# Performance work log

Measured on AMD Instinct MI355X. Metric: run time of the kernel, lower is better.

Reference implementation:

```python
import jax, jax.numpy as jnp
import numpy as np

NUM_FILTER = 256
CAPS_LEN = 8
NUM_EMOTIONS = 8
OUT_DIM = 16
NUM_CHANNEL = 25
TIME_LEN = 25
NUM_CAPS = NUM_CHANNEL * TIME_LEN * (NUM_FILTER // CAPS_LEN)  # 20000
NUM_ITERATIONS = 3


def setup_inputs() -> dict:
    key = jax.random.key(0)
    ks = jax.random.split(key, 10)
    B = 32
    x = jax.random.normal(ks[0], (B, 54, 54), jnp.float32)
    conv1_w = jax.random.normal(ks[1], (NUM_FILTER, 1, 6, 6), jnp.float32) * 0.05
    conv1_b = jax.random.normal(ks[2], (NUM_FILTER,), jnp.float32) * 0.01
    conv2_w = jax.random.normal(ks[3], (NUM_FILTER, NUM_FILTER, 6, 6), jnp.float32) * 0.01
    conv2_b = jax.random.normal(ks[4], (NUM_FILTER,), jnp.float32) * 0.01
    conv3_w = jax.random.normal(ks[5], (NUM_FILTER, 2 * NUM_FILTER, 1, 1), jnp.float32) * 0.05
    conv3_b = jax.random.normal(ks[6], (NUM_FILTER,), jnp.float32) * 0.01
    # PrimaryCaps: one Linear(caps_len -> caps_len) per capsule, batched as [nc, out, in]
    pc_w = jax.random.normal(ks[7], (NUM_CAPS, CAPS_LEN, CAPS_LEN), jnp.float32) * 0.1
    pc_b = jax.random.normal(ks[8], (NUM_CAPS, CAPS_LEN), jnp.float32) * 0.1
    # EmotionCaps transform W: [nc, num_emotions, out_dim, in_dim]
    W = jax.random.normal(ks[9], (NUM_CAPS, NUM_EMOTIONS, OUT_DIM, CAPS_LEN), jnp.float32) * 0.05
    return {"x": x, "conv1_w": conv1_w, "conv1_b": conv1_b, "conv2_w": conv2_w,
            "conv2_b": conv2_b, "conv3_w": conv3_w, "conv3_b": conv3_b,
            "pc_w": pc_w, "pc_b": pc_b, "W": W}


def _conv(x, w, b, stride):
    y = jax.lax.conv_general_dilated(x, w, (stride, stride), 'VALID',
                                     dimension_numbers=('NCHW', 'OIHW', 'NCHW'))
    return y + b[None, :, None, None]


def _squash(s):
    # scale = |s|^2 / (1 + |s|^2); out = scale * s / (|s| + 1e-8)
    n2 = jnp.sum(s * s, axis=-1, keepdims=True)
    n = jnp.sqrt(n2)
    return (n2 / (1.0 + n2)) * s / (n + 1e-8)


def reference(x, conv1_w, conv1_b, conv2_w, conv2_b, conv3_w, conv3_b, pc_w, pc_b, W):
    x4 = x[:, None]                                    # [B,1,54,54]
    x1 = jax.nn.relu(_conv(x4, conv1_w, conv1_b, 2))   # [B,F,25,25]
    y = jnp.pad(x1, ((0, 0), (0, 0), (2, 3), (2, 3)))  # ZeroPad2d((2,3,2,3))
    y = jax.nn.relu(_conv(y, conv2_w, conv2_b, 1))     # [B,F,25,25]
    z = jax.nn.relu(jnp.concatenate([x1, y], axis=1))  # [B,2F,25,25]
    z = _conv(z, conv3_w, conv3_b, 1)                  # [B,F,25,25]
    B, F, H, Wd = z.shape
    # flatten to capsules: [B, F//caps_len, caps_len, H*W] -> [B, nc, caps_len]
    caps = z.reshape(B, F // CAPS_LEN, CAPS_LEN, H * Wd)
    caps = caps.transpose(0, 1, 3, 2).reshape(B, NUM_CAPS, CAPS_LEN)
    # PrimaryCaps: per-capsule linear, batched as a single einsum
    u = jnp.einsum('bni,noi->bno', caps, pc_w) + pc_b[None]   # [B,nc,caps_len]
    # EmotionCaps: u_hat[b,n,e,o] = W[n,e,o,i] u[b,n,i]
    u_hat = jnp.einsum('bni,neoi->bneo', u, W)                # [B,nc,ne,out_dim]
    b = jnp.zeros((B, NUM_CAPS, NUM_EMOTIONS), u.dtype)
    v = None
    for r in range(NUM_ITERATIONS):
        c = jax.nn.softmax(b, axis=2)[..., None]              # [B,nc,ne,1]
        v = _squash(jnp.sum(c * u_hat, axis=1))               # [B,ne,out_dim]
        if r < NUM_ITERATIONS - 1:
            b = b + jnp.einsum('bneo,beo->bne', u_hat, v)
    return jnp.linalg.norm(v, axis=-1)                        # [B,ne]
```

## Files before the change

kernel.cpp:

```cpp
#include <hip/hip_runtime.h>
#include <hip/hip_fp16.h>

typedef unsigned short u16;
typedef __attribute__((ext_vector_type(8))) short bf16x8;
typedef __attribute__((ext_vector_type(4))) float floatx4;
typedef __attribute__((ext_vector_type(2))) _Float16 half2v;

#define NPIX 625
#define NCAPS 20000
#define K2 9216

__device__ __forceinline__ u16 f2bf(float f) {
  unsigned u = __float_as_uint(f);
  return (u16)((u + 0x7fffu + ((u >> 16) & 1u)) >> 16);
}

__device__ __forceinline__ unsigned h16(float f) {
  union { _Float16 h; u16 b; } c;
  c.h = (_Float16)f;
  return (unsigned)c.b;
}

__device__ __forceinline__ half2v as_h2(unsigned u) {
  union { unsigned i; half2v h; } c;
  c.i = u;
  return c.h;
}

__device__ __forceinline__ float dot2f(unsigned a, unsigned b, float c) {
#if __has_builtin(__builtin_amdgcn_fdot2)
  return __builtin_amdgcn_fdot2(as_h2(a), as_h2(b), c, false);
#else
  half2v x = as_h2(a), y = as_h2(b);
  return fmaf((float)x[1], (float)y[1], fmaf((float)x[0], (float)y[0], c));
#endif
}

__device__ __forceinline__ float dotrow16(uint4 w, uint4 u) {
  float s = dot2f(w.x, u.x, 0.f);
  s = dot2f(w.y, u.y, s);
  s = dot2f(w.z, u.z, s);
  s = dot2f(w.w, u.w, s);
  return s;
}

__device__ __forceinline__ float dot8v(float4 a0, float4 a1, float4 b0, float4 b1) {
  float s = a0.x * b0.x;
  s = fmaf(a0.y, b0.y, s); s = fmaf(a0.z, b0.z, s); s = fmaf(a0.w, b0.w, s);
  s = fmaf(a1.x, b1.x, s); s = fmaf(a1.y, b1.y, s);
  s = fmaf(a1.z, b1.z, s); s = fmaf(a1.w, b1.w, s);
  return s;
}

#define GLDS16(g, l) __builtin_amdgcn_global_load_lds( \
    (const __attribute__((address_space(1))) void*)(g), \
    (__attribute__((address_space(3))) void*)(l), 16, 0, 0)

#define MFMA16(a, b, c) __builtin_amdgcn_mfma_f32_16x16x32_bf16((a), (b), (c), 0, 0, 0)

__global__ void prep_conv1(const float* __restrict__ w2, const float* __restrict__ w3,
                           u16* __restrict__ A2c, u16* __restrict__ A3,
                           const float* __restrict__ x, const float* __restrict__ w1,
                           const float* __restrict__ b1, u16* __restrict__ x1p) {
  if (blockIdx.x < 256) {
    const int oc = blockIdx.x, c = threadIdx.x;
    const float* src = w2 + (oc * 256 + c) * 36;
    float v[36];
#pragma unroll
    for (int k = 0; k < 9; k++) {
      const float4 q = *(const float4*)(src + k * 4);
      v[k * 4 + 0] = q.x; v[k * 4 + 1] = q.y; v[k * 4 + 2] = q.z; v[k * 4 + 3] = q.w;
    }
#pragma unroll
    for (int g = 0; g < 36; g++) {
      const int ktp = g / 9, tl = g % 9;
      A2c[(ktp * 256 + oc) * 2304 + tl * 256 + c] = f2bf(v[g]);
    }
  } else if (blockIdx.x < 384) {
    const int j = (blockIdx.x - 256) * 1024 + threadIdx.x * 4;
    const float4 q = *(const float4*)(w3 + j);
    ushort4 p;
    p.x = f2bf(q.x); p.y = f2bf(q.y); p.z = f2bf(q.z); p.w = f2bf(q.w);
    *(ushort4*)(A3 + j) = p;
  } else {
    const int blk = blockIdx.x - 384;
    const int b = blk / 25, i = blk % 25;
    const int f = threadIdx.x;
    float wreg[36];
#pragma unroll
    for (int k = 0; k < 36; k++) wreg[k] = w1[f * 36 + k];
    float bias = b1[f];
    const float* xb = x + b * 54 * 54 + (2 * i) * 54;
    for (int j = 0; j < 25; j++) {
      float acc = bias;
#pragma unroll
      for (int ki = 0; ki < 6; ki++)
#pragma unroll
        for (int kj = 0; kj < 6; kj++)
          acc = fmaf(xb[ki * 54 + 2 * j + kj], wreg[ki * 6 + kj], acc);
      x1p[(((b * 30 + i + 2) * 30) + (j + 2)) * 256 + f] = f2bf(fmaxf(acc, 0.f));
    }
  }
}

__global__ __launch_bounds__(512, 1) void conv2_gemm(const u16* __restrict__ A2n,
    const u16* __restrict__ x1p, u16* __restrict__ P) {
  __shared__ __align__(16) u16 lds[2][36864];
  const int tid = threadIdx.x;
  const int lane = tid & 63, wave = tid >> 6;
  const int bid = blockIdx.x;
  const int xcd = bid & 7, idx = bid >> 3;
  const int kt = xcd & 3;
  const int ntile = (xcd >> 2) ? (32 + idx) : idx;
  const int wm = wave & 1, wn = wave >> 1;
  const int lrow = lane & 15, kg = lane >> 4;

  const int trow = tid >> 3;
  const int xoff = 8 * ((tid & 7) ^ (trow & 7));
  const u16* aSrc = A2n + (kt * 256 + trow) * 2304 + xoff;
  const int nb = ntile * 320;
  auto pixrow = [&](int r) {
    int n = nb + r;
    if (n > NCAPS - 1) n = NCAPS - 1;
    const int b = n / NPIX, p = n % NPIX;
    const int i = p / 25, j = p % 25;
    return ((b * 30 + i) * 30 + j) * 256;
  };
  const u16* bSrc0 = x1p + pixrow(trow) + xoff;
  const u16* bSrc1 = x1p + pixrow(64 + trow) + xoff;
  const u16* bSrc2 = x1p + pixrow(128 + trow) + xoff;
  const u16* bSrc3 = x1p + pixrow(192 + trow) + xoff;
  const u16* bSrc4 = x1p + pixrow(256 + trow) + xoff;

  auto stageA = [&](u16* L, int tt) {
    const u16* a = aSrc + tt * 64;
    GLDS16(a,               L + tid * 8);
    GLDS16(a + 64 * 2304,   L + 4096 + tid * 8);
    GLDS16(a + 128 * 2304,  L + 8192 + tid * 8);
    GLDS16(a + 192 * 2304,  L + 12288 + tid * 8);
  };
  auto stageB = [&](u16* L, int tt) {
    const int g = kt * 9 + (tt >> 2);
    const int boff = ((g / 6) * 30 + (g % 6)) * 256 + (tt & 3) * 64;
    GLDS16(bSrc0 + boff, L + 16384 + tid * 8);
    GLDS16(bSrc1 + boff, L + 20480 + tid * 8);
    GLDS16(bSrc2 + boff, L + 24576 + tid * 8);
    GLDS16(bSrc3 + boff, L + 28672 + tid * 8);
    GLDS16(bSrc4 + boff, L + 32768 + tid * 8);
  };

  floatx4 acc[8][5] = {};
  const int jx0 = 8 * (kg ^ (lrow & 7));
  const int jx1 = 8 * ((4 + kg) ^ (lrow & 7));
  const int arow = wm * 128 + lrow;
  const int brow = wn * 80 + lrow;

  stageA(lds[0], 0);
  stageB(lds[0], 0);
  asm volatile("s_waitcnt vmcnt(0)" ::: "memory");
  __builtin_amdgcn_s_barrier();

  for (int t = 0; t < 36; t++) {
    u16* Cur = lds[t & 1];
    u16* Oth = lds[(t & 1) ^ 1];
    const bool st = (t < 35);
    bf16x8 af[4], bv[5];

#pragma unroll
    for (int fm = 0; fm < 4; fm++)
      af[fm] = *(const bf16x8*)(Cur + (arow + fm * 16) * 64 + jx0);
#pragma unroll
    for (int fn = 0; fn < 5; fn++)
      bv[fn] = *(const bf16x8*)(Cur + 16384 + (brow + fn * 16) * 64 + jx0);
    if (st) { stageA(Oth, t + 1); stageB(Oth, t + 1); }
    asm volatile("" ::: "memory");
    __builtin_amdgcn_s_barrier();
    __builtin_amdgcn_s_setprio(1);
#pragma unroll
    for (int fm = 0; fm < 4; fm++)
#pragma unroll
      for (int fn = 0; fn < 5; fn++)
        acc[fm][fn] = MFMA16(af[fm], bv[fn], acc[fm][fn]);
    __builtin_amdgcn_s_setprio(0);
    __builtin_amdgcn_sched_barrier(0);
    __builtin_amdgcn_s_barrier();

    bf16x8 ag[4];
#pragma unroll
    for (int fm = 0; fm < 4; fm++)
      ag[fm] = *(const bf16x8*)(Cur + (arow + 64 + fm * 16) * 64 + jx0);
    asm volatile("" ::: "memory");
    __builtin_amdgcn_s_barrier();
    __builtin_amdgcn_s_setprio(1);
#pragma unroll
    for (int fm = 0; fm < 4; fm++)
#pragma unroll
      for (int fn = 0; fn < 5; fn++)
        acc[4 + fm][fn] = MFMA16(ag[fm], bv[fn], acc[4 + fm][fn]);
    __builtin_amdgcn_s_setprio(0);
    __builtin_amdgcn_sched_barrier(0);
    __builtin_amdgcn_s_barrier();

#pragma unroll
    for (int fm = 0; fm < 4; fm++)
      af[fm] = *(const bf16x8*)(Cur + (arow + fm * 16) * 64 + jx1);
#pragma unroll
    for (int fn = 0; fn < 5; fn++)
      bv[fn] = *(const bf16x8*)(Cur + 16384 + (brow + fn * 16) * 64 + jx1);
    asm volatile("" ::: "memory");
    __builtin_amdgcn_s_barrier();
    __builtin_amdgcn_s_setprio(1);
#pragma unroll
    for (int fm = 0; fm < 4; fm++)
#pragma unroll
      for (int fn = 0; fn < 5; fn++)
        acc[fm][fn] = MFMA16(af[fm], bv[fn], acc[fm][fn]);
    __builtin_amdgcn_s_setprio(0);
    __builtin_amdgcn_sched_barrier(0);
    __builtin_amdgcn_s_barrier();

#pragma unroll
    for (int fm = 0; fm < 4; fm++)
      ag[fm] = *(const bf16x8*)(Cur + (arow + 64 + fm * 16) * 64 + jx1);
    asm volatile("" ::: "memory");
    __builtin_amdgcn_s_barrier();
    __builtin_amdgcn_s_setprio(1);
#pragma unroll
    for (int fm = 0; fm < 4; fm++)
#pragma unroll
      for (int fn = 0; fn < 5; fn++)
        acc[4 + fm][fn] = MFMA16(ag[fm], bv[fn], acc[4 + fm][fn]);
    __builtin_amdgcn_s_setprio(0);
    __builtin_amdgcn_sched_barrier(0);
    asm volatile("s_waitcnt vmcnt(0)" ::: "memory");
    __builtin_amdgcn_sched_barrier(0);
    __builtin_amdgcn_s_barrier();
  }

  u16* Pk = P + kt * 5120000;
#pragma unroll
  for (int fn = 0; fn < 5; fn++) {
    const int n = nb + wn * 80 + fn * 16 + lrow;
    if (n < NCAPS) {
#pragma unroll
      for (int fm = 0; fm < 8; fm++) {
        const int oc = wm * 128 + fm * 16 + kg * 4;
        ushort4 pk;
        pk.x = f2bf(acc[fm][fn][0]);
        pk.y = f2bf(acc[fm][fn][1]);
        pk.z = f2bf(acc[fm][fn][2]);
        pk.w = f2bf(acc[fm][fn][3]);
        *(ushort4*)(Pk + n * 256 + oc) = pk;
      }
    }
  }
}

__global__ void conv2_red(const u16* __restrict__ P, const float* __restrict__ bias2,
                          u16* __restrict__ y) {
  const int idx = blockIdx.x * 256 + threadIdx.x;
  const ushort4 p0 = *(const ushort4*)(P + idx * 4);
  const ushort4 p1 = *(const ushort4*)(P + 5120000 + idx * 4);
  const ushort4 p2 = *(const ushort4*)(P + 10240000 + idx * 4);
  const ushort4 p3 = *(const ushort4*)(P + 15360000 + idx * 4);
  const float4 bs = *(const float4*)(bias2 + ((idx * 4) & 255));
  auto bf = [](unsigned v) { return __uint_as_float(v << 16); };
  float sx = bf(p0.x) + bf(p1.x) + bf(p2.x) + bf(p3.x) + bs.x;
  float sy = bf(p0.y) + bf(p1.y) + bf(p2.y) + bf(p3.y) + bs.y;
  float sz = bf(p0.z) + bf(p1.z) + bf(p2.z) + bf(p3.z) + bs.z;
  float sw = bf(p0.w) + bf(p1.w) + bf(p2.w) + bf(p3.w) + bs.w;
  ushort4 pk;
  pk.x = f2bf(fmaxf(sx, 0.f));
  pk.y = f2bf(fmaxf(sy, 0.f));
  pk.z = f2bf(fmaxf(sz, 0.f));
  pk.w = f2bf(fmaxf(sw, 0.f));
  *(ushort4*)(y + idx * 4) = pk;
}

__global__ __launch_bounds__(256) void conv3_gemm(const u16* __restrict__ A3,
    const u16* __restrict__ x1p, const u16* __restrict__ y, u16* __restrict__ P3) {
  __shared__ u16 As[128 * 32];
  __shared__ u16 Bs[128 * 32];
  const int tid = threadIdx.x;
  const int lane = tid & 63, wave = tid >> 6;
  const int mtile = blockIdx.x, ntile = blockIdx.y, kt = blockIdx.z;

  const int seg0 = tid, seg1 = tid + 256;
  const u16* ga0 = A3 + (mtile * 128 + (seg0 >> 2)) * 512 + (seg0 & 3) * 8 + kt * 256;
  const u16* ga1 = A3 + (mtile * 128 + (seg1 >> 2)) * 512 + (seg1 & 3) * 8 + kt * 256;

  auto mkbase = [&](int seg) {
    int n = ntile * 128 + (seg >> 2);
    if (n > NCAPS - 1) n = NCAPS - 1;
    if (kt == 0) {
      int b = n / NPIX, p = n % NPIX;
      int i = p / 25, j = p % 25;
      return x1p + ((b * 30 + i + 2) * 30 + (j + 2)) * 256 + (seg & 3) * 8;
    }
    return y + n * 256 + (seg & 3) * 8;
  };
  const u16* gs0 = mkbase(seg0);
  const u16* gs1 = mkbase(seg1);

  floatx4 acc[4][4] = {};
  const int wm = wave & 1, wn = wave >> 1;
  const int lrow = lane & 15, kgrp = lane >> 4;

  for (int kc = 0; kc < 8; kc++) {
    GLDS16(ga0 + kc * 32, As + seg0 * 8);
    GLDS16(ga1 + kc * 32, As + seg1 * 8);
    GLDS16(gs0 + kc * 32, Bs + seg0 * 8);
    GLDS16(gs1 + kc * 32, Bs + seg1 * 8);
    __syncthreads();
    bf16x8 af[4], bfr[4];
#pragma unroll
    for (int tt = 0; tt < 4; tt++) {
      af[tt]  = *(const bf16x8*)(As + (wm * 64 + tt * 16 + lrow) * 32 + kgrp * 8);
      bfr[tt] = *(const bf16x8*)(Bs + (wn * 64 + tt * 16 + lrow) * 32 + kgrp * 8);
    }
#pragma unroll
    for (int tm = 0; tm < 4; tm++)
#pragma unroll
      for (int tn = 0; tn < 4; tn++)
        acc[tm][tn] = __builtin_amdgcn_mfma_f32_16x16x32_bf16(af[tm], bfr[tn], acc[tm][tn], 0, 0, 0);
    __syncthreads();
  }

  u16* Pk = P3 + kt * 5120000;
  const int nb = ntile * 128 + wn * 64;
  const int fb = mtile * 128 + wm * 64 + kgrp * 4;
#pragma unroll
  for (int tn = 0; tn < 4; tn++) {
    int n = nb + tn * 16 + lrow;
    if (n < NCAPS) {
#pragma unroll
      for (int tm = 0; tm < 4; tm++) {
        int f0 = fb + tm * 16;
        ushort4 pk;
        pk.x = f2bf(acc[tm][tn][0]);
        pk.y = f2bf(acc[tm][tn][1]);
        pk.z = f2bf(acc[tm][tn][2]);
        pk.w = f2bf(acc[tm][tn][3]);
        *(ushort4*)(Pk + n * 256 + f0) = pk;
      }
    }
  }
}

__global__ void prep_caps(const float* __restrict__ W, u16* __restrict__ Wbs,
                          const u16* __restrict__ P3, const float* __restrict__ b3,
                          const float* __restrict__ pcw, const float* __restrict__ pcb,
                          unsigned* __restrict__ u2) {
  const int tid = threadIdx.x;
  if (blockIdx.x < 10000) {
    int r = blockIdx.x * 256 + tid;
    int n = r >> 7, eo = r & 127;
    int e = eo >> 4, o = eo & 15;
    const float* src = W + n * 1024 + eo * 8;
    const float4 v0 = *(const float4*)src;
    const float4 v1 = *(const float4*)(src + 4);
    u16* dst = Wbs + n * 1088 + e * 136 + o * 8;
    ushort4 p0, p1;
    p0.x = (u16)h16(v0.x); p0.y = (u16)h16(v0.y); p0.z = (u16)h16(v0.z); p0.w = (u16)h16(v0.w);
    p1.x = (u16)h16(v1.x); p1.y = (u16)h16(v1.y); p1.z = (u16)h16(v1.z); p1.w = (u16)h16(v1.w);
    *(ushort4*)dst = p0;
    *(ushort4*)(dst + 4) = p1;
  } else {
    const int blk = blockIdx.x - 10000;
    const int b = tid >> 3, o = tid & 7;
    for (int k = 0; k < 8; k++) {
      const int n = blk * 8 + k;
      const int g = n / NPIX, p = n % NPIX;
      const u16* pa = P3 + ((b * NPIX + p) * 256 + g * 8);
      const uint4 qa = *(const uint4*)pa;
      const uint4 qb = *(const uint4*)(pa + 5120000);
      const float* bp = b3 + g * 8;
      const float4 bb0 = *(const float4*)bp;
      const float4 bb1 = *(const float4*)(bp + 4);
      float4 c0, c1;
      c0.x = __uint_as_float(qa.x << 16) + __uint_as_float(qb.x << 16) + bb0.x;
      c0.y = __uint_as_float(qa.x & 0xffff0000u) + __uint_as_float(qb.x & 0xffff0000u) + bb0.y;
      c0.z = __uint_as_float(qa.y << 16) + __uint_as_float(qb.y << 16) + bb0.z;
      c0.w = __uint_as_float(qa.y & 0xffff0000u) + __uint_as_float(qb.y & 0xffff0000u) + bb0.w;
      c1.x = __uint_as_float(qa.z << 16) + __uint_as_float(qb.z << 16) + bb1.x;
      c1.y = __uint_as_float(qa.z & 0xffff0000u) + __uint_as_float(qb.z & 0xffff0000u) + bb1.y;
      c1.z = __uint_as_float(qa.w << 16) + __uint_as_float(qb.w << 16) + bb1.z;
      c1.w = __uint_as_float(qa.w & 0xffff0000u) + __uint_as_float(qb.w & 0xffff0000u) + bb1.w;
      const float* pw = pcw + n * 64 + o * 8;
      float4 w0 = *(const float4*)pw;
      float4 w1 = *(const float4*)(pw + 4);
      const float myu = pcb[n * 8 + o] + dot8v(w0, w1, c0, c1);
      const float partner = __shfl_xor(myu, 1, 64);
      if (!(o & 1)) {
        unsigned pk = h16(myu) | (h16(partner) << 16);
        u2[n * 128 + b * 4 + (o >> 1)] = pk;
      }
    }
  }
}

__global__ __launch_bounds__(256, 4) void caps_accb2(const unsigned* __restrict__ u2,
    const u16* __restrict__ Wbs, const float* __restrict__ vsum,
    float* __restrict__ Spart, int zero_v) {
  __shared__ u16 Ws[16 * 1088];
  const int tid = threadIdx.x;
  const int b = tid >> 3, e = tid & 7;
  const int n0 = blockIdx.x * 16;

  const u16* gsrc = Wbs + n0 * 1088;
#pragma unroll
  for (int k = 0; k < 9; k++) {
    const int idx = k * 256 + tid;
    if (idx < 2176) GLDS16(gsrc + idx * 8, Ws + idx * 8);
  }

  float4 V0 = make_float4(0.f, 0.f, 0.f, 0.f), V1 = V0, V2 = V0, V3 = V0;
  if (!zero_v) {
    const float* vp = vsum + tid * 16;
    V0 = *(const float4*)vp;
    V1 = *(const float4*)(vp + 4);
    V2 = *(const float4*)(vp + 8);
    V3 = *(const float4*)(vp + 12);
  }
  float s0 = 0.f, s1 = 0.f, s2 = 0.f, s3 = 0.f, s4 = 0.f, s5 = 0.f, s6 = 0.f, s7 = 0.f;
  float s8 = 0.f, s9 = 0.f, s10 = 0.f, s11 = 0.f, s12 = 0.f, s13 = 0.f, s14 = 0.f, s15 = 0.f;

  __syncthreads();

  for (int it = 0; it < 16; it++) {
    const int n = n0 + it;
    const uint4 up = *(const uint4*)(u2 + n * 128 + b * 4);
    const u16* Wn = Ws + it * 1088 + e * 136;
    float h0, h1, h2, h3, h4, h5, h6, h7, h8, h9, h10, h11, h12, h13, h14, h15;
#define ROW(o, H) { uint4 w = *(const uint4*)(Wn + (o) * 8); H = dotrow16(w, up); }
    ROW(0, h0)   ROW(1, h1)   ROW(2, h2)   ROW(3, h3)
    ROW(4, h4)   ROW(5, h5)   ROW(6, h6)   ROW(7, h7)
    ROW(8, h8)   ROW(9, h9)   ROW(10, h10) ROW(11, h11)
    ROW(12, h12) ROW(13, h13) ROW(14, h14) ROW(15, h15)
#undef ROW
    float c;
    if (zero_v) {
      c = 0.125f;
    } else {
      float blog = h0 * V0.x;
      blog = fmaf(h1, V0.y, blog);  blog = fmaf(h2, V0.z, blog);  blog = fmaf(h3, V0.w, blog);
      blog = fmaf(h4, V1.x, blog);  blog = fmaf(h5, V1.y, blog);  blog = fmaf(h6, V1.z, blog);
      blog = fmaf(h7, V1.w, blog);  blog = fmaf(h8, V2.x, blog);  blog = fmaf(h9, V2.y, blog);
      blog = fmaf(h10, V2.z, blog); blog = fmaf(h11, V2.w, blog); blog = fmaf(h12, V3.x, blog);
      blog = fmaf(h13, V3.y, blog); blog = fmaf(h14, V3.z, blog); blog = fmaf(h15, V3.w, blog);
      float m = blog;
      m = fmaxf(m, __shfl_xor(m, 1, 64));
      m = fmaxf(m, __shfl_xor(m, 2, 64));
      m = fmaxf(m, __shfl_xor(m, 4, 64));
      float ex = __expf(blog - m);
      float ss = ex;
      ss += __shfl_xor(ss, 1, 64);
      ss += __shfl_xor(ss, 2, 64);
      ss += __shfl_xor(ss, 4, 64);
      c = ex / ss;
    }
    s0 = fmaf(c, h0, s0);   s1 = fmaf(c, h1, s1);   s2 = fmaf(c, h2, s2);   s3 = fmaf(c, h3, s3);
    s4 = fmaf(c, h4, s4);   s5 = fmaf(c, h5, s5);   s6 = fmaf(c, h6, s6);   s7 = fmaf(c, h7, s7);
    s8 = fmaf(c, h8, s8);   s9 = fmaf(c, h9, s9);   s10 = fmaf(c, h10, s10); s11 = fmaf(c, h11, s11);
    s12 = fmaf(c, h12, s12); s13 = fmaf(c, h13, s13); s14 = fmaf(c, h14, s14); s15 = fmaf(c, h15, s15);
  }
  float* Sp = Spart + blockIdx.x * 4096 + tid * 16;
  *(float4*)(Sp + 0)  = make_float4(s0, s1, s2, s3);
  *(float4*)(Sp + 4)  = make_float4(s4, s5, s6, s7);
  *(float4*)(Sp + 8)  = make_float4(s8, s9, s10, s11);
  *(float4*)(Sp + 12) = make_float4(s12, s13, s14, s15);
}

__global__ void caps_redB(const float* __restrict__ Spart, float* __restrict__ Sp2) {
  const int j = blockIdx.x * 256 + threadIdx.x;
  const int r0 = blockIdx.y * 50;
  float a0 = 0.f, a1 = 0.f;
  for (int r = 0; r < 50; r += 2) {
    a0 += Spart[(r0 + r) * 4096 + j];
    a1 += Spart[(r0 + r + 1) * 4096 + j];
  }
  Sp2[blockIdx.y * 4096 + j] = a0 + a1;
}

__global__ void caps_v2(const float* __restrict__ Sp2, float* __restrict__ vsum, int add) {
  const int t = threadIdx.x;
  float4 a0 = make_float4(0.f, 0.f, 0.f, 0.f), a1 = a0, a2 = a0, a3 = a0;
  for (int r = 0; r < 25; r++) {
    const float* sp = Sp2 + r * 4096 + t * 16;
    const float4 q0 = *(const float4*)sp;
    const float4 q1 = *(const float4*)(sp + 4);
    const float4 q2 = *(const float4*)(sp + 8);
    const float4 q3 = *(const float4*)(sp + 12);
    a0.x += q0.x; a0.y += q0.y; a0.z += q0.z; a0.w += q0.w;
    a1.x += q1.x; a1.y += q1.y; a1.z += q1.z; a1.w += q1.w;
    a2.x += q2.x; a2.y += q2.y; a2.z += q2.z; a2.w += q2.w;
    a3.x += q3.x; a3.y += q3.y; a3.z += q3.z; a3.w += q3.w;
  }
  float n2 = a0.x * a0.x;
  n2 = fmaf(a0.y, a0.y, n2); n2 = fmaf(a0.z, a0.z, n2); n2 = fmaf(a0.w, a0.w, n2);
  n2 = fmaf(a1.x, a1.x, n2); n2 = fmaf(a1.y, a1.y, n2); n2 = fmaf(a1.z, a1.z, n2); n2 = fmaf(a1.w, a1.w, n2);
  n2 = fmaf(a2.x, a2.x, n2); n2 = fmaf(a2.y, a2.y, n2); n2 = fmaf(a2.z, a2.z, n2); n2 = fmaf(a2.w, a2.w, n2);
  n2 = fmaf(a3.x, a3.x, n2); n2 = fmaf(a3.y, a3.y, n2); n2 = fmaf(a3.z, a3.z, n2); n2 = fmaf(a3.w, a3.w, n2);
  const float n = sqrtf(n2);
  const float scale = n2 / ((1.f + n2) * (n + 1e-8f));
  float* vp = vsum + t * 16;
  float4 o0, o1, o2, o3;
  if (add) {
    o0 = *(float4*)(vp + 0); o1 = *(float4*)(vp + 4); o2 = *(float4*)(vp + 8); o3 = *(float4*)(vp + 12);
  } else {
    o0 = make_float4(0.f, 0.f, 0.f, 0.f); o1 = o0; o2 = o0; o3 = o0;
  }
  o0.x = fmaf(a0.x, scale, o0.x); o0.y = fmaf(a0.y, scale, o0.y);
  o0.z = fmaf(a0.z, scale, o0.z); o0.w = fmaf(a0.w, scale, o0.w);
  o1.x = fmaf(a1.x, scale, o1.x); o1.y = fmaf(a1.y, scale, o1.y);
  o1.z = fmaf(a1.z, scale, o1.z); o1.w = fmaf(a1.w, scale, o1.w);
  o2.x = fmaf(a2.x, scale, o2.x); o2.y = fmaf(a2.y, scale, o2.y);
  o2.z = fmaf(a2.z, scale, o2.z); o2.w = fmaf(a2.w, scale, o2.w);
  o3.x = fmaf(a3.x, scale, o3.x); o3.y = fmaf(a3.y, scale, o3.y);
  o3.z = fmaf(a3.z, scale, o3.z); o3.w = fmaf(a3.w, scale, o3.w);
  *(float4*)(vp + 0) = o0; *(float4*)(vp + 4) = o1;
  *(float4*)(vp + 8) = o2; *(float4*)(vp + 12) = o3;
}

__global__ void caps_out2(const float* __restrict__ Sp2, float* __restrict__ out) {
  const int t = threadIdx.x;
  float4 a0 = make_float4(0.f, 0.f, 0.f, 0.f), a1 = a0, a2 = a0, a3 = a0;
  for (int r = 0; r < 25; r++) {
    const float* sp = Sp2 + r * 4096 + t * 16;
    const float4 q0 = *(const float4*)sp;
    const float4 q1 = *(const float4*)(sp + 4);
    const float4 q2 = *(const float4*)(sp + 8);
    const float4 q3 = *(const float4*)(sp + 12);
    a0.x += q0.x; a0.y += q0.y; a0.z += q0.z; a0.w += q0.w;
    a1.x += q1.x; a1.y += q1.y; a1.z += q1.z; a1.w += q1.w;
    a2.x += q2.x; a2.y += q2.y; a2.z += q2.z; a2.w += q2.w;
    a3.x += q3.x; a3.y += q3.y; a3.z += q3.z; a3.w += q3.w;
  }
  float n2 = a0.x * a0.x;
  n2 = fmaf(a0.y, a0.y, n2); n2 = fmaf(a0.z, a0.z, n2); n2 = fmaf(a0.w, a0.w, n2);
  n2 = fmaf(a1.x, a1.x, n2); n2 = fmaf(a1.y, a1.y, n2); n2 = fmaf(a1.z, a1.z, n2); n2 = fmaf(a1.w, a1.w, n2);
  n2 = fmaf(a2.x, a2.x, n2); n2 = fmaf(a2.y, a2.y, n2); n2 = fmaf(a2.z, a2.z, n2); n2 = fmaf(a2.w, a2.w, n2);
  n2 = fmaf(a3.x, a3.x, n2); n2 = fmaf(a3.y, a3.y, n2); n2 = fmaf(a3.z, a3.z, n2); n2 = fmaf(a3.w, a3.w, n2);
  const float n = sqrtf(n2);
  out[t] = n * n2 / ((1.f + n2) * (n + 1e-8f));
}

extern "C" void kernel_launch(void* const* d_in, const int* in_sizes, int n_in,
                              void* d_out, int out_size, void* d_ws, size_t ws_size,
                              hipStream_t stream) {
  const float* x   = (const float*)d_in[0];
  const float* w1  = (const float*)d_in[1];
  const float* b1  = (const float*)d_in[2];
  const float* w2  = (const float*)d_in[3];
  const float* b2  = (const float*)d_in[4];
  const float* w3  = (const float*)d_in[5];
  const float* b3  = (const float*)d_in[6];
  const float* pcw = (const float*)d_in[7];
  const float* pcb = (const float*)d_in[8];
  const float* W   = (const float*)d_in[9];
  float* out = (float*)d_out;

  char* ws = (char*)d_ws;

  u16*   x1p = (u16*)(ws + 0);
  u16*   A2  = (u16*)(ws + 14745600);
  u16*   A3  = (u16*)(ws + 19464192);
  u16*   y   = (u16*)(ws + 19726336);
  u16*   P   = (u16*)(ws + 29966336);
  u16*   P3  = (u16*)(ws + 43520000);
  u16*   Wbs = (u16*)(ws + 0);
  float* Spart = (float*)(ws + 43520000);
  unsigned* u2 = (unsigned*)(ws + 64000000);
  float* Sp2 = (float*)(ws + 74240000);
  float* vs  = (float*)(ws + 74649600);

  hipMemsetAsync(x1p, 0, 14745600, stream);

  prep_conv1<<<1184, 256, 0, stream>>>(w2, w3, A2, A3, x, w1, b1, x1p);
  conv2_gemm<<<252, 512, 0, stream>>>(A2, x1p, P);
  conv2_red<<<5000, 256, 0, stream>>>(P, b2, y);
  conv3_gemm<<<dim3(2, 157, 2), 256, 0, stream>>>(A3, x1p, y, P3);
  prep_caps<<<12500, 256, 0, stream>>>(W, Wbs, P3, b3, pcw, pcb, u2);

  for (int pass = 0; pass < 3; pass++) {
    caps_accb2<<<1250, 256, 0, stream>>>(u2, Wbs, vs, Spart, pass == 0 ? 1 : 0);
    caps_redB<<<dim3(16, 25), 256, 0, stream>>>(Spart, Sp2);
    if (pass == 0)      caps_v2<<<1, 256, 0, stream>>>(Sp2, vs, 0);
    else if (pass == 1) caps_v2<<<1, 256, 0, stream>>>(Sp2, vs, 1);
    else                caps_out2<<<1, 256, 0, stream>>>(Sp2, out);
  }
}
```

Baseline: 442.1 us.

## Software-pipeline LDS fragment reads and drop per-phase barriers in conv2 GEMM

The main MFMA loop is restructured so that the first A/B fragments of the next K-tile are read from LDS right after the single end-of-iteration barrier. The remaining fragment reads are interleaved ahead of each MFMA group. The four intra-iteration s_barrier calls and the s_setprio toggles are removed, leaving one wait-and-barrier per tile. This aims to cut synchronization stalls and hide LDS latency behind MFMAs, at the cost of more live fragment registers (af, bvA, bvB, ag, af2, ag2), which may raise VGPR pressure.

Measured after the change: 425.6 us (median of 2 runs). 3.7% less time.

```diff
diff --git a/kernel.cpp b/kernel.cpp
--- a/kernel.cpp
+++ b/kernel.cpp
@@ -155,86 +155,76 @@
   const int arow = wm * 128 + lrow;
   const int brow = wn * 80 + lrow;
 
+  auto rdA = [&](const u16* L, int row, int jx) {
+    return *(const bf16x8*)(L + row * 64 + jx);
+  };
+  auto rdB = [&](const u16* L, int row, int jx) {
+    return *(const bf16x8*)(L + 16384 + row * 64 + jx);
+  };
+
   stageA(lds[0], 0);
   stageB(lds[0], 0);
   asm volatile("s_waitcnt vmcnt(0)" ::: "memory");
   __builtin_amdgcn_s_barrier();
 
+  bf16x8 af[4], bvA[5];
+#pragma unroll
+  for (int fm = 0; fm < 4; fm++) af[fm] = rdA(lds[0], arow + fm * 16, jx0);
+#pragma unroll
+  for (int fn = 0; fn < 5; fn++) bvA[fn] = rdB(lds[0], brow + fn * 16, jx0);
+
   for (int t = 0; t < 36; t++) {
     u16* Cur = lds[t & 1];
     u16* Oth = lds[(t & 1) ^ 1];
     const bool st = (t < 35);
-    bf16x8 af[4], bv[5];
-
+
+    if (st) { stageA(Oth, t + 1); stageB(Oth, t + 1); }
+    bf16x8 ag[4], bvB[5];
+#pragma unroll
+    for (int fm = 0; fm < 4; fm++) ag[fm] = rdA(Cur, arow + 64 + fm * 16, jx0);
+#pragma unroll
+    for (int fn = 0; fn < 5; fn++) bvB[fn] = rdB(Cur, brow + fn * 16, jx1);
 #pragma unroll
     for (int fm = 0; fm < 4; fm++)
-      af[fm] = *(const bf16x8*)(Cur + (arow + fm * 16) * 64 + jx0);
-#pragma unroll
-    for (int fn = 0; fn < 5; fn++)
-      bv[fn] = *(const bf16x8*)(Cur + 16384 + (brow + fn * 16) * 64 + jx0);
-    if (st) { stageA(Oth, t + 1); stageB(Oth, t + 1); }
-    asm volatile("" ::: "memory");
-    __builtin_amdgcn_s_barrier();
-    __builtin_amdgcn_s_setprio(1);
+#pragma unroll
+      for (int fn = 0; fn < 5; fn++)
+        acc[fm][fn] = MFMA16(af[fm], bvA[fn], acc[fm][fn]);
+    __builtin_amdgcn_sched_barrier(0);
+
+    bf16x8 af2[4];
+#pragma unroll
+    for (int fm = 0; fm < 4; fm++) af2[fm] = rdA(Cur, arow + fm * 16, jx1);
 #pragma unroll
     for (int fm = 0; fm < 4; fm++)
 #pragma unroll
       for (int fn = 0; fn < 5; fn++)
-        acc[fm][fn] = MFMA16(af[fm], bv[fn], acc[fm][fn]);
-    __builtin_amdgcn_s_setprio(0);
+        acc[4 + fm][fn] = MFMA16(ag[fm], bvA[fn], acc[4 + fm][fn]);
     __builtin_amdgcn_sched_barrier(0);
-    __builtin_amdgcn_s_barrier();
-
-    bf16x8 ag[4];
+
+    bf16x8 ag2[4];
+#pragma unroll
+    for (int fm = 0; fm < 4; fm++) ag2[fm] = rdA(Cur, arow + 64 + fm * 16, jx1);
 #pragma unroll
     for (int fm = 0; fm < 4; fm++)
-      ag[fm] = *(const bf16x8*)(Cur + (arow + 64 + fm * 16) * 64 + jx0);
-    asm volatile("" ::: "memory");
-    __builtin_amdgcn_s_barrier();
-    __builtin_amdgcn_s_setprio(1);
+#pragma unroll
+      for (int fn = 0; fn < 5; fn++)
+        acc[fm][fn] = MFMA16(af2[fm], bvB[fn], acc[fm][fn]);
+    __builtin_amdgcn_sched_barrier(0);
+
 #pragma unroll
     for (int fm = 0; fm < 4; fm++)
 #pragma unroll
       for (int fn = 0; fn < 5; fn++)
-        acc[4 + fm][fn] = MFMA16(ag[fm], bv[fn], acc[4 + fm][fn]);
-    __builtin_amdgcn_s_setprio(0);
-    __builtin_amdgcn_sched_barrier(0);
-    __builtin_amdgcn_s_barrier();
-
-#pragma unroll
-    for (int fm = 0; fm < 4; fm++)
-      af[fm] = *(const bf16x8*)(Cur + (arow + fm * 16) * 64 + jx1);
-#pragma unroll
-    for (int fn = 0; fn < 5; fn++)
-      bv[fn] = *(const bf16x8*)(Cur + 16384 + (brow + fn * 16) * 64 + jx1);
-    asm volatile("" ::: "memory");
-    __builtin_amdgcn_s_barrier();
-    __builtin_amdgcn_s_setprio(1);
-#pragma unroll
-    for (int fm = 0; fm < 4; fm++)
-#pragma unroll
-      for (int fn = 0; fn < 5; fn++)
-        acc[fm][fn] = MFMA16(af[fm], bv[fn], acc[fm][fn]);
-    __builtin_amdgcn_s_setprio(0);
-    __builtin_amdgcn_sched_barrier(0);
-    __builtin_amdgcn_s_barrier();
-
-#pragma unroll
-    for (int fm = 0; fm < 4; fm++)
-      ag[fm] = *(const bf16x8*)(Cur + (arow + 64 + fm * 16) * 64 + jx1);
-    asm volatile("" ::: "memory");
-    __builtin_amdgcn_s_barrier();
-    __builtin_amdgcn_s_setprio(1);
-#pragma unroll
-    for (int fm = 0; fm < 4; fm++)
-#pragma unroll
-      for (int fn = 0; fn < 5; fn++)
-        acc[4 + fm][fn] = MFMA16(ag[fm], bv[fn], acc[4 + fm][fn]);
-    __builtin_amdgcn_s_setprio(0);
-    __builtin_amdgcn_sched_barrier(0);
-    asm volatile("s_waitcnt vmcnt(0)" ::: "memory");
-    __builtin_amdgcn_sched_barrier(0);
-    __builtin_amdgcn_s_barrier();
+        acc[4 + fm][fn] = MFMA16(ag2[fm], bvB[fn], acc[4 + fm][fn]);
+
+    if (st) {
+      asm volatile("s_waitcnt vmcnt(0)" ::: "memory");
+      __builtin_amdgcn_s_barrier();
+#pragma unroll
+      for (int fm = 0; fm < 4; fm++) af[fm] = rdA(Oth, arow + fm * 16, jx0);
+#pragma unroll
+      for (int fn = 0; fn < 5; fn++) bvA[fn] = rdB(Oth, brow + fn * 16, jx0);
+    }
   }
 
   u16* Pk = P + kt * 5120000;
```
